# Kernel optimization log

Hardware: AMD Instinct MI355X
Metric: run time of the kernel (lower is better)

## Reference

```python
import jax, jax.numpy as jnp
import numpy as np


def setup_inputs() -> dict:
    key = jax.random.key(0)
    k1, k2, k3, k4 = jax.random.split(key, 4)
    B, S, IN, OUT = 4, 2048, 4096, 16384
    inp = jax.random.normal(k1, (B, S, IN), dtype=jnp.float32)
    # int8-range quantized weights stored as int32 (stand-in for torch int8)
    quant_w = jax.random.randint(k2, (OUT, IN), -127, 128, dtype=jnp.int32)
    # per-output-row dequant scale (abs-max / 127 style): small positive
    scale_w = jax.random.uniform(k3, (OUT,), dtype=jnp.float32) * 0.02 + 1e-4
    bias = jax.random.normal(k4, (OUT,), dtype=jnp.float32)
    return {"inp": inp, "quant_w": quant_w, "scale_w": scale_w, "bias": bias,
            "weight_bit_width": 8}


def reference(inp, quant_w, scale_w, bias, weight_bit_width):
    # extract_weight_to_half: dequantize per-row scaled int8 weights (8-bit path)
    weight = quant_w.astype(scale_w.dtype) * scale_w[:, None]  # [OUT, IN]
    # inp.view(-1, IN).mm(weight.t()) -> [..., OUT], then add bias
    out = jnp.einsum('bsi,oi->bso', inp, weight) + bias
    return out
```

## Files before the change

### kernel.cpp

```cpp
#include <hip/hip_runtime.h>
#include <stdint.h>


typedef unsigned short u16;
using frag_t = __attribute__((ext_vector_type(8))) short;
using f32x4  = __attribute__((ext_vector_type(4))) float;
using u16x8  = __attribute__((ext_vector_type(8))) u16;

#define BM 256
#define BN 256
#define BK 64
#define HB 8192

#define VMW(n) asm volatile("s_waitcnt vmcnt(" #n ")" ::: "memory")
#define BAR()  asm volatile("s_barrier" ::: "memory")

__device__ __forceinline__ void gld_lds16(const void* g, void* l) {
    __builtin_amdgcn_global_load_lds(
        (const __attribute__((address_space(1))) void*)g,
        (__attribute__((address_space(3))) void*)l,
        16, 0, 0);
}

__device__ __forceinline__ u16 f2bf(float f) {
    uint32_t u = __builtin_bit_cast(uint32_t, f);
    u += 0x7fffu + ((u >> 16) & 1u);
    return (u16)(u >> 16);
}

__global__ void cvt_f32_to_bf16(const float* __restrict__ in,
                                u16* __restrict__ out, long n8) {
    long i = (long)blockIdx.x * blockDim.x + threadIdx.x;
    if (i >= n8) return;
    long base = i * 8;
    const float4* p = (const float4*)(in + base);
    float4 f0 = p[0], f1 = p[1];
    u16x8 o;
    o[0] = f2bf(f0.x); o[1] = f2bf(f0.y); o[2] = f2bf(f0.z); o[3] = f2bf(f0.w);
    o[4] = f2bf(f1.x); o[5] = f2bf(f1.y); o[6] = f2bf(f1.z); o[7] = f2bf(f1.w);
    *(u16x8*)(out + base) = o;
}

__global__ void cvt_i32_to_bf16(const int* __restrict__ in,
                                u16* __restrict__ out, long n8) {
    long i = (long)blockIdx.x * blockDim.x + threadIdx.x;
    if (i >= n8) return;
    long base = i * 8;
    const int4* p = (const int4*)(in + base);
    int4 a = p[0], b = p[1];
    u16x8 o;
    o[0] = f2bf((float)a.x); o[1] = f2bf((float)a.y);
    o[2] = f2bf((float)a.z); o[3] = f2bf((float)a.w);
    o[4] = f2bf((float)b.x); o[5] = f2bf((float)b.y);
    o[6] = f2bf((float)b.z); o[7] = f2bf((float)b.w);
    *(u16x8*)(out + base) = o;
}

__global__ __launch_bounds__(512, 2)
void gemm256(const u16* __restrict__ A, const u16* __restrict__ B,
             const float* __restrict__ scale, const float* __restrict__ bias,
             float* __restrict__ C, int M, int N, int K) {
    extern __shared__ u16 lds[];
    u16* As = lds;
    u16* Bs = lds + 4 * HB;

    const int tid  = threadIdx.x;
    const int wv   = tid >> 6;
    const int lane = tid & 63;
    const int wm   = wv >> 2;
    const int wn   = wv & 3;

    const int nbx = N / BN;
    const int nwg = (M / BM) * nbx;
    const int cpx = nwg >> 3;
    const int gid = blockIdx.x;
    const int wg  = (gid & 7) * cpx + (gid >> 3);
    const long row0 = (long)(wg / nbx) * BM;
    const long col0 = (long)(wg % nbx) * BN;
    const int NT = K / BK;

    const int r0 = (wv * 2 + 0) * 8 + (lane >> 3);
    const int r1 = (wv * 2 + 1) * 8 + (lane >> 3);
    const int sl = lane & 7;
    const u16* a0 = A + (row0 + ((r0 >> 6) * 128 + (r0 & 63))) * (long)K + ((sl ^ (r0 & 7)) << 3);
    const u16* a1 = A + (row0 + ((r1 >> 6) * 128 + (r1 & 63))) * (long)K + ((sl ^ (r1 & 7)) << 3);
    const u16* b0 = B + (col0 + ((r0 >> 5) * 64 + (r0 & 31))) * (long)K + ((sl ^ (r0 & 7)) << 3);
    const u16* b1 = B + (col0 + ((r1 >> 5) * 64 + (r1 & 31))) * (long)K + ((sl ^ (r1 & 7)) << 3);
    const int d0 = (wv * 2 + 0) * 512;
    const int d1 = (wv * 2 + 1) * 512;

    const int frow = lane & 15;
    const int kgrp = lane >> 4;
    const int oe0  = frow * 64 + (((kgrp    ) ^ (frow & 7)) << 3);
    const int oe1  = frow * 64 + (((kgrp + 4) ^ (frow & 7)) << 3);

    f32x4  acc[8][4] = {};
    frag_t af[4][2];
    frag_t bf[2][2][2];

#define STAGE_A(th, qm, bufq) do {                                   \
    u16* dst = As + ((bufq) * 2 + (qm)) * HB;                        \
    const long ko = (long)(th) * BK + (long)(qm) * 64 * K;           \
    gld_lds16(a0 + ko, dst + d0);                                    \
    gld_lds16(a1 + ko, dst + d1); } while (0)

#define STAGE_B(th, qn, bufq) do {                                   \
    u16* dst = Bs + ((bufq) * 2 + (qn)) * HB;                        \
    const long ko = (long)(th) * BK + (long)(qn) * 32 * K;           \
    gld_lds16(b0 + ko, dst + d0);                                    \
    gld_lds16(b1 + ko, dst + d1); } while (0)

#define LOAD_A(qm, bufq) do {                                        \
    const u16* p = As + ((bufq) * 2 + (qm)) * HB + wm * 64 * 64;     \
    _Pragma("unroll") for (int i = 0; i < 4; ++i) {                  \
        af[i][0] = *(const frag_t*)(p + i * 16 * 64 + oe0);          \
        af[i][1] = *(const frag_t*)(p + i * 16 * 64 + oe1); } } while (0)

#define LOAD_B(qn, bufq) do {                                        \
    const u16* p = Bs + ((bufq) * 2 + (qn)) * HB + wn * 32 * 64;     \
    _Pragma("unroll") for (int j = 0; j < 2; ++j) {                  \
        bf[qn][j][0] = *(const frag_t*)(p + j * 16 * 64 + oe0);      \
        bf[qn][j][1] = *(const frag_t*)(p + j * 16 * 64 + oe1); } } while (0)

#define MFMA_Q(qm, qn) do {                                          \
    __builtin_amdgcn_s_setprio(1);                                   \
    _Pragma("unroll") for (int i = 0; i < 4; ++i)                    \
    _Pragma("unroll") for (int j = 0; j < 2; ++j) {                  \
        acc[(qm)*4+i][(qn)*2+j] = __builtin_amdgcn_mfma_f32_16x16x32_bf16( \
            af[i][0], bf[qn][j][0], acc[(qm)*4+i][(qn)*2+j], 0, 0, 0);     \
        acc[(qm)*4+i][(qn)*2+j] = __builtin_amdgcn_mfma_f32_16x16x32_bf16( \
            af[i][1], bf[qn][j][1], acc[(qm)*4+i][(qn)*2+j], 0, 0, 0); }   \
    __builtin_amdgcn_s_setprio(0); } while (0)

    STAGE_A(0, 0, 0); STAGE_B(0, 0, 0); STAGE_B(0, 1, 0); STAGE_A(0, 1, 0);
    STAGE_A(1, 0, 1); STAGE_B(1, 0, 1);

    int T = 0;
    for (; T < NT - 2; ++T) {
        const int buf = T & 1;
        VMW(8); BAR();
        LOAD_A(0, buf); LOAD_B(0, buf);
        STAGE_B(T + 1, 1, buf ^ 1);
        MFMA_Q(0, 0);
        VMW(8); BAR();
        LOAD_B(1, buf);
        STAGE_A(T + 1, 1, buf ^ 1);
        MFMA_Q(0, 1);
        VMW(8); BAR();
        LOAD_A(1, buf);
        STAGE_A(T + 2, 0, buf);
        MFMA_Q(1, 1);
        STAGE_B(T + 2, 0, buf);
        MFMA_Q(1, 0);
    }
    {
        const int buf = T & 1;
        VMW(8); BAR();
        LOAD_A(0, buf); LOAD_B(0, buf);
        STAGE_B(T + 1, 1, buf ^ 1);
        MFMA_Q(0, 0);
        VMW(8); BAR();
        LOAD_B(1, buf);
        STAGE_A(T + 1, 1, buf ^ 1);
        MFMA_Q(0, 1);
        VMW(8); BAR();
        LOAD_A(1, buf);
        MFMA_Q(1, 1);
        MFMA_Q(1, 0);
        ++T;
    }
    {
        const int buf = T & 1;
        VMW(4); BAR();
        LOAD_A(0, buf); LOAD_B(0, buf);
        MFMA_Q(0, 0);
        VMW(2); BAR();
        LOAD_B(1, buf);
        MFMA_Q(0, 1);
        VMW(0); BAR();
        LOAD_A(1, buf);
        MFMA_Q(1, 1);
        MFMA_Q(1, 0);
    }

    const int crow = (lane >> 4) * 4;
    const int ccol = lane & 15;
    const long orow = row0 + wm * 128;
    const long ocol = col0 + wn * 64 + ccol;
    float sc[4], bi[4];
#pragma unroll
    for (int j = 0; j < 4; ++j) {
        sc[j] = scale[ocol + j * 16];
        bi[j] = bias[ocol + j * 16];
    }
#pragma unroll
    for (int i = 0; i < 8; ++i) {
#pragma unroll
        for (int r = 0; r < 4; ++r) {
            float* cp = C + (orow + i * 16 + crow + r) * (long)N + ocol;
#pragma unroll
            for (int j = 0; j < 4; ++j)
                cp[j * 16] = acc[i][j][r] * sc[j] + bi[j];
        }
    }
#undef STAGE_A
#undef STAGE_B
#undef LOAD_A
#undef LOAD_B
#undef MFMA_Q
}

extern "C" void kernel_launch(void* const* d_in, const int* in_sizes, int n_in,
                              void* d_out, int out_size, void* d_ws, size_t ws_size,
                              hipStream_t stream) {
    const float* inp   = (const float*)d_in[0];
    const int*   qw    = (const int*)d_in[1];
    const float* scale = (const float*)d_in[2];
    const float* bias  = (const float*)d_in[3];

    const long n_inp = (long)in_sizes[0];
    const long n_w   = (long)in_sizes[1];
    const int  N     = in_sizes[2];
    const int  K     = (int)(n_w / N);
    const int  M     = (int)(n_inp / K);

    u16* a_bf = (u16*)d_ws;
    u16* b_bf = (u16*)d_ws + n_inp;

    {
        long n8 = n_inp / 8;
        cvt_f32_to_bf16<<<(int)((n8 + 255) / 256), 256, 0, stream>>>(inp, a_bf, n8);
    }
    {
        long n8 = n_w / 8;
        cvt_i32_to_bf16<<<(int)((n8 + 255) / 256), 256, 0, stream>>>(qw, b_bf, n8);
    }

    static int attr_set = 0;
    if (!attr_set) {
        hipFuncSetAttribute((const void*)gemm256,
                            hipFuncAttributeMaxDynamicSharedMemorySize, 131072);
        attr_set = 1;
    }
    const int nwg = (M / BM) * (N / BN);
    gemm256<<<nwg, 512, 131072, stream>>>(a_bf, b_bf, scale, bias,
                                          (float*)d_out, M, N, K);
}
```

Before: 1.594 ms.

## Double-buffer A/B register fragments and prefetch next tile's first quadrant early

Splits the register fragments into separate A0/A1 and B0/B1 sets so LDS reads for the next k-tile's first quadrant are issued at the end of the current iteration, overlapping with the tail MFMAs. It also reorders the MFMA loop to iterate k-halves outermost, which spaces out dependent accumulations. This adds register pressure (an extra A fragment set) under the 2-waves-per-SIMD launch bound and shifts the barrier/wait points, which risks spills or changed waitcnt correctness.

```diff
diff --git a/kernel.cpp b/kernel.cpp
--- a/kernel.cpp
+++ b/kernel.cpp
@@ -95,8 +95,8 @@
     const int oe1  = frow * 64 + (((kgrp + 4) ^ (frow & 7)) << 3);
 
     f32x4  acc[8][4] = {};
-    frag_t af[4][2];
-    frag_t bf[2][2][2];
+    frag_t A0[4][2], A1[4][2];
+    frag_t B0[2][2], B1[2][2];
 
 #define STAGE_A(th, qm, bufq) do {                                   \
     u16* dst = As + ((bufq) * 2 + (qm)) * HB;                        \
@@ -110,77 +110,76 @@
     gld_lds16(b0 + ko, dst + d0);                                    \
     gld_lds16(b1 + ko, dst + d1); } while (0)
 
-#define LOAD_A(qm, bufq) do {                                        \
+#define LOAD_A(dst, qm, bufq) do {                                   \
     const u16* p = As + ((bufq) * 2 + (qm)) * HB + wm * 64 * 64;     \
     _Pragma("unroll") for (int i = 0; i < 4; ++i) {                  \
-        af[i][0] = *(const frag_t*)(p + i * 16 * 64 + oe0);          \
-        af[i][1] = *(const frag_t*)(p + i * 16 * 64 + oe1); } } while (0)
-
-#define LOAD_B(qn, bufq) do {                                        \
+        dst[i][0] = *(const frag_t*)(p + i * 16 * 64 + oe0);         \
+        dst[i][1] = *(const frag_t*)(p + i * 16 * 64 + oe1); } } while (0)
+
+#define LOAD_B(dst, qn, bufq) do {                                   \
     const u16* p = Bs + ((bufq) * 2 + (qn)) * HB + wn * 32 * 64;     \
     _Pragma("unroll") for (int j = 0; j < 2; ++j) {                  \
-        bf[qn][j][0] = *(const frag_t*)(p + j * 16 * 64 + oe0);      \
-        bf[qn][j][1] = *(const frag_t*)(p + j * 16 * 64 + oe1); } } while (0)
-
-#define MFMA_Q(qm, qn) do {                                          \
+        dst[j][0] = *(const frag_t*)(p + j * 16 * 64 + oe0);         \
+        dst[j][1] = *(const frag_t*)(p + j * 16 * 64 + oe1); } } while (0)
+
+#define MFMA_Q(qm, qn, AF, BF) do {                                  \
     __builtin_amdgcn_s_setprio(1);                                   \
+    _Pragma("unroll") for (int kk = 0; kk < 2; ++kk)                 \
     _Pragma("unroll") for (int i = 0; i < 4; ++i)                    \
-    _Pragma("unroll") for (int j = 0; j < 2; ++j) {                  \
+    _Pragma("unroll") for (int j = 0; j < 2; ++j)                    \
         acc[(qm)*4+i][(qn)*2+j] = __builtin_amdgcn_mfma_f32_16x16x32_bf16( \
-            af[i][0], bf[qn][j][0], acc[(qm)*4+i][(qn)*2+j], 0, 0, 0);     \
-        acc[(qm)*4+i][(qn)*2+j] = __builtin_amdgcn_mfma_f32_16x16x32_bf16( \
-            af[i][1], bf[qn][j][1], acc[(qm)*4+i][(qn)*2+j], 0, 0, 0); }   \
+            AF[i][kk], BF[j][kk], acc[(qm)*4+i][(qn)*2+j], 0, 0, 0);       \
     __builtin_amdgcn_s_setprio(0); } while (0)
 
     STAGE_A(0, 0, 0); STAGE_B(0, 0, 0); STAGE_B(0, 1, 0); STAGE_A(0, 1, 0);
     STAGE_A(1, 0, 1); STAGE_B(1, 0, 1);
+    VMW(8); BAR();
+    LOAD_A(A0, 0, 0); LOAD_B(B0, 0, 0);
 
     int T = 0;
     for (; T < NT - 2; ++T) {
         const int buf = T & 1;
-        VMW(8); BAR();
-        LOAD_A(0, buf); LOAD_B(0, buf);
         STAGE_B(T + 1, 1, buf ^ 1);
-        MFMA_Q(0, 0);
-        VMW(8); BAR();
-        LOAD_B(1, buf);
+        MFMA_Q(0, 0, A0, B0);
+        VMW(8); BAR();
+        LOAD_B(B1, 1, buf);
         STAGE_A(T + 1, 1, buf ^ 1);
-        MFMA_Q(0, 1);
-        VMW(8); BAR();
-        LOAD_A(1, buf);
+        MFMA_Q(0, 1, A0, B1);
+        VMW(8); BAR();
+        LOAD_A(A1, 1, buf);
         STAGE_A(T + 2, 0, buf);
-        MFMA_Q(1, 1);
+        MFMA_Q(1, 1, A1, B1);
         STAGE_B(T + 2, 0, buf);
-        MFMA_Q(1, 0);
+        MFMA_Q(1, 0, A1, B0);
+        VMW(8); BAR();
+        LOAD_A(A0, 0, buf ^ 1); LOAD_B(B0, 0, buf ^ 1);
     }
     {
         const int buf = T & 1;
-        VMW(8); BAR();
-        LOAD_A(0, buf); LOAD_B(0, buf);
         STAGE_B(T + 1, 1, buf ^ 1);
-        MFMA_Q(0, 0);
-        VMW(8); BAR();
-        LOAD_B(1, buf);
+        MFMA_Q(0, 0, A0, B0);
+        VMW(8); BAR();
+        LOAD_B(B1, 1, buf);
         STAGE_A(T + 1, 1, buf ^ 1);
-        MFMA_Q(0, 1);
-        VMW(8); BAR();
-        LOAD_A(1, buf);
-        MFMA_Q(1, 1);
-        MFMA_Q(1, 0);
+        MFMA_Q(0, 1, A0, B1);
+        VMW(8); BAR();
+        LOAD_A(A1, 1, buf);
+        MFMA_Q(1, 1, A1, B1);
+        MFMA_Q(1, 0, A1, B0);
+        VMW(4); BAR();
+        LOAD_A(A0, 0, buf ^ 1); LOAD_B(B0, 0, buf ^ 1);
         ++T;
     }
     {
         const int buf = T & 1;
-        VMW(4); BAR();
-        LOAD_A(0, buf); LOAD_B(0, buf);
-        MFMA_Q(0, 0);
+        MFMA_Q(0, 0, A0, B0);
         VMW(2); BAR();
-        LOAD_B(1, buf);
-        MFMA_Q(0, 1);
+        LOAD_B(B1, 1, buf);
+        MFMA_Q(0, 1, A0, B1);
         VMW(0); BAR();
-        LOAD_A(1, buf);
-        MFMA_Q(1, 1);
-        MFMA_Q(1, 0);
+        LOAD_A(A1, 1, buf);
+        MFMA_Q(1, 1, A1, B1);
+        MFMA_Q(1, 0, A1, B0);
     }
 
     const int crow = (lane >> 4) * 4;
```

After: 1.620 ms. About the same (+1.7%).
